# Kernel optimization log

Measured on AMD Instinct MI355X. Metric: run time of the kernel, lower is better.

The kernel has to match this reference:

```python
import jax, jax.numpy as jnp
import numpy as np

B, S, D, H, T, R = 2, 2048, 768, 12, 64, 50
DH = D // H
EPS = 1e-12


def setup_inputs() -> dict:
    key = jax.random.key(0)
    ks = jax.random.split(key, 12)
    w = lambda k, shape: jax.random.normal(k, shape, jnp.float32) * 0.02
    inp = {
        "hidden_states": jax.random.normal(ks[0], (B, S, D), jnp.float32),
        "tag_emb": w(ks[1], (T, D)),
        "sa_wq": w(ks[2], (D, D)), "sa_bq": jnp.zeros((D,), jnp.float32),
        "sa_wk": w(ks[3], (D, D)), "sa_bk": jnp.zeros((D,), jnp.float32),
        "sa_wv": w(ks[4], (D, D)), "sa_bv": jnp.zeros((D,), jnp.float32),
        "sa_wo": w(ks[5], (D, D)), "sa_bo": jnp.zeros((D,), jnp.float32),
        "sa_ln_g": jnp.ones((D,), jnp.float32), "sa_ln_b": jnp.zeros((D,), jnp.float32),
        "ca_wq": w(ks[6], (D, D)), "ca_bq": jnp.zeros((D,), jnp.float32),
        "ca_wk": w(ks[7], (D, D)), "ca_bk": jnp.zeros((D,), jnp.float32),
        "ca_wv": w(ks[8], (D, D)), "ca_bv": jnp.zeros((D,), jnp.float32),
        "ca_wo": w(ks[9], (D, D)), "ca_bo": jnp.zeros((D,), jnp.float32),
        "ca_ln_g": jnp.ones((D,), jnp.float32), "ca_ln_b": jnp.zeros((D,), jnp.float32),
        "ff_w1": w(ks[10], (D, 3072)), "ff_b1": jnp.zeros((3072,), jnp.float32),
        "ff_w2": w(ks[11], (3072, D)), "ff_b2": jnp.zeros((D,), jnp.float32),
        "ff_ln_g": jnp.ones((D,), jnp.float32), "ff_ln_b": jnp.zeros((D,), jnp.float32),
    }
    return inp


def _layernorm(x, g, b):
    m = jnp.mean(x, axis=-1, keepdims=True)
    v = jnp.mean(jnp.square(x - m), axis=-1, keepdims=True)
    return (x - m) * jax.lax.rsqrt(v + EPS) * g + b


def _bert_attention(x, kv, mask, wq, bq, wk, bk, wv, bv, wo, bo, ln_g, ln_b):
    # BertSelfAttention: multi-head attn; mask (if any) is ADDED to scores (HF semantics).
    Bq, Sq = x.shape[0], x.shape[1]
    Sk = kv.shape[1]
    q = (x @ wq + bq).reshape(Bq, Sq, H, DH)
    k = (kv @ wk + bk).reshape(Bq, Sk, H, DH)
    v = (kv @ wv + bv).reshape(Bq, Sk, H, DH)
    scores = jnp.einsum("bqhd,bkhd->bhqk", q, k) / jnp.sqrt(jnp.float32(DH))
    if mask is not None:
        scores = scores + mask  # additive 0/1 band mask, as in the source
    probs = jax.nn.softmax(scores, axis=-1)
    ctx = jnp.einsum("bhqk,bkhd->bqhd", probs, v).reshape(Bq, Sq, D)
    # BertSelfOutput: dense + residual + LayerNorm
    return _layernorm(ctx @ wo + bo + x, ln_g, ln_b)


def reference(hidden_states, tag_emb,
              sa_wq, sa_bq, sa_wk, sa_bk, sa_wv, sa_bv, sa_wo, sa_bo, sa_ln_g, sa_ln_b,
              ca_wq, ca_bq, ca_wk, ca_bk, ca_wv, ca_bv, ca_wo, ca_bo, ca_ln_g, ca_ln_b,
              ff_w1, ff_b1, ff_w2, ff_b2, ff_ln_g, ff_ln_b):
    Sd = hidden_states.shape[1]
    # banded mask: tril(+R) * triu(-R) -> 1 inside window, 0 outside (added to scores)
    i = jnp.arange(Sd)
    band = (jnp.abs(i[:, None] - i[None, :]) <= R).astype(hidden_states.dtype)  # [S,S]
    attn_out = _bert_attention(hidden_states, hidden_states, band,
                               sa_wq, sa_bq, sa_wk, sa_bk, sa_wv, sa_bv,
                               sa_wo, sa_bo, sa_ln_g, sa_ln_b)
    tags = jnp.broadcast_to(tag_emb[None], (hidden_states.shape[0], T, D))
    attn_out = _bert_attention(attn_out, tags, None,
                               ca_wq, ca_bq, ca_wk, ca_bk, ca_wv, ca_bv,
                               ca_wo, ca_bo, ca_ln_g, ca_ln_b)
    # BertIntermediate + BertOutput (exact erf gelu as in HF)
    inter = jax.nn.gelu(attn_out @ ff_w1 + ff_b1, approximate=False)
    return _layernorm(inter @ ff_w2 + ff_b2 + attn_out, ff_ln_g, ff_ln_b)
```

## Files before the change

kernel.cpp:

```cpp
#include <hip/hip_runtime.h>
#include <cstdint>
#include <cstddef>


typedef __bf16 bf16;
typedef __bf16 bf16x8 __attribute__((ext_vector_type(8)));
typedef __bf16 bf16x4 __attribute__((ext_vector_type(4)));
typedef __bf16 bf16x2 __attribute__((ext_vector_type(2)));
typedef float  floatx4 __attribute__((ext_vector_type(4)));

__device__ __forceinline__ void glds16(const bf16* g, bf16* l) {
  __builtin_amdgcn_global_load_lds((const __attribute__((address_space(1))) void*)g,
                                   (__attribute__((address_space(3))) void*)l, 16, 0, 0);
}

__device__ __forceinline__ float fexp2(float x) {
  float r;
  asm("v_exp_f32 %0, %1" : "=v"(r) : "v"(x));
  return r;
}

__global__ __launch_bounds__(256) void k_concat3(const float* __restrict__ a,
                                                 const float* __restrict__ b,
                                                 const float* __restrict__ c,
                                                 float* __restrict__ o, int seg) {
  int i = blockIdx.x * 256 + threadIdx.x;
  int s = i / seg, j = i - s * seg;
  const float* p = s == 0 ? a : (s == 1 ? b : c);
  o[i] = p[j];
}

__global__ void k_pad_tags(const float* __restrict__ tag, bf16* __restrict__ out) {
  int i = blockIdx.x * 256 + threadIdx.x;
  if (i < 64 * 768) out[i] = (bf16)tag[i];
  else if (i < 128 * 768) out[i] = (bf16)0.f;
}

__global__ __launch_bounds__(256) void k_transpose(const float* __restrict__ W,
                                                   bf16* __restrict__ Wt,
                                                   int K, int N) {
  __shared__ bf16 tile[64][72];
  int n0 = blockIdx.x * 64, k0 = blockIdx.y * 64;
  int t = threadIdx.x;
  int r = t >> 2, cg = (t & 3) * 16;
  const float* src = W + (size_t)(k0 + r) * N + n0 + cg;
  float tmp[16];
  *(float4*)&tmp[0]  = *(const float4*)(src);
  *(float4*)&tmp[4]  = *(const float4*)(src + 4);
  *(float4*)&tmp[8]  = *(const float4*)(src + 8);
  *(float4*)&tmp[12] = *(const float4*)(src + 12);
#pragma unroll
  for (int i = 0; i < 16; ++i) tile[r][cg + i] = (bf16)tmp[i];
  __syncthreads();
  bf16* dst = Wt + (size_t)(n0 + r) * K + k0 + cg;
#pragma unroll
  for (int g = 0; g < 2; ++g) {
    bf16x8 pack;
#pragma unroll
    for (int i = 0; i < 8; ++i) pack[i] = tile[cg + g * 8 + i][r];
    *(bf16x8*)(dst + g * 8) = pack;
  }
}

__global__ __launch_bounds__(256) void k_transpose4(const float* __restrict__ W0,
                                                    const float* __restrict__ W1,
                                                    const float* __restrict__ W2w,
                                                    const float* __restrict__ W3,
                                                    bf16* __restrict__ Wt) {
  __shared__ bf16 tile[64][72];
  int z = blockIdx.z;
  const float* W = z == 0 ? W0 : (z == 1 ? W1 : (z == 2 ? W2w : W3));
  bf16* dstb = Wt + (size_t)z * 768 * 768;
  int n0 = blockIdx.x * 64, k0 = blockIdx.y * 64;
  int t = threadIdx.x;
  int r = t >> 2, cg = (t & 3) * 16;
  const float* src = W + (size_t)(k0 + r) * 768 + n0 + cg;
  float tmp[16];
  *(float4*)&tmp[0]  = *(const float4*)(src);
  *(float4*)&tmp[4]  = *(const float4*)(src + 4);
  *(float4*)&tmp[8]  = *(const float4*)(src + 8);
  *(float4*)&tmp[12] = *(const float4*)(src + 12);
#pragma unroll
  for (int i = 0; i < 16; ++i) tile[r][cg + i] = (bf16)tmp[i];
  __syncthreads();
  bf16* dst = dstb + (size_t)(n0 + r) * 768 + k0 + cg;
#pragma unroll
  for (int g = 0; g < 2; ++g) {
    bf16x8 pack;
#pragma unroll
    for (int i = 0; i < 8; ++i) pack[i] = tile[cg + g * 8 + i][r];
    *(bf16x8*)(dst + g * 8) = pack;
  }
}

template <int BM, int KS, bool AF32, bool CF32>
__global__ __launch_bounds__(256) void k_gemm(const void* __restrict__ Av,
                                              const bf16* __restrict__ Bt,
                                              const float* __restrict__ bias,
                                              void* __restrict__ Cv,
                                              int M, int N, int K, int act) {
  constexpr int MT = BM / 32;
  __shared__ bf16 As[KS][BM * 32];
  __shared__ bf16 Bs[KS][128 * 32];
  int tid = threadIdx.x;
  int lane = tid & 63, wave = tid >> 6;
  int l16 = lane & 15, quad = lane >> 4;
  int wm = wave & 1, wn = wave >> 1;
  int m0 = blockIdx.x * BM, n0 = blockIdx.y * 128;
  int arow = tid >> 2, acol = (tid & 3) * 8;
  int ldst = arow * 32 + acol;

  const bf16* Ab = (const bf16*)Av;
  const float* Af = (const float*)Av;
  const bf16* Ap = Ab + (size_t)(m0 + arow) * K + acol;
  const float* Apf = Af + (size_t)(m0 + arow) * K + acol;
  const bf16* Bp = Bt + (size_t)(n0 + arow) * K + acol;

  floatx4 acc[MT][4];
#pragma unroll
  for (int i = 0; i < MT; ++i)
#pragma unroll
    for (int j = 0; j < 4; ++j) acc[i][j] = floatx4{0.f, 0.f, 0.f, 0.f};

  float4 p0a, p0b, p1a, p1b;
  if constexpr (AF32) {
    p0a = *(const float4*)(Apf);
    p0b = *(const float4*)(Apf + 4);
    p1a = *(const float4*)(Apf + (size_t)64 * K);
    p1b = *(const float4*)(Apf + (size_t)64 * K + 4);
  }

  for (int k = 0; k < K; k += 32 * KS) {
    __syncthreads();
#pragma unroll
    for (int ks = 0; ks < KS; ++ks) {
      glds16(Bp + k + ks * 32, &Bs[ks][ldst]);
      glds16(Bp + (size_t)64 * K + k + ks * 32, &Bs[ks][ldst + 2048]);
    }
    if constexpr (AF32) {
      bf16x8 c0, c1;
      c0[0] = (bf16)p0a.x; c0[1] = (bf16)p0a.y; c0[2] = (bf16)p0a.z; c0[3] = (bf16)p0a.w;
      c0[4] = (bf16)p0b.x; c0[5] = (bf16)p0b.y; c0[6] = (bf16)p0b.z; c0[7] = (bf16)p0b.w;
      c1[0] = (bf16)p1a.x; c1[1] = (bf16)p1a.y; c1[2] = (bf16)p1a.z; c1[3] = (bf16)p1a.w;
      c1[4] = (bf16)p1b.x; c1[5] = (bf16)p1b.y; c1[6] = (bf16)p1b.z; c1[7] = (bf16)p1b.w;
      *(bf16x8*)&As[0][ldst] = c0;
      *(bf16x8*)&As[0][ldst + 2048] = c1;
    } else {
#pragma unroll
      for (int ks = 0; ks < KS; ++ks) {
        glds16(Ap + k + ks * 32, &As[ks][ldst]);
        if constexpr (BM == 128) glds16(Ap + (size_t)64 * K + k + ks * 32, &As[ks][ldst + 2048]);
      }
    }
    __syncthreads();
    if constexpr (AF32) {
      if (k + 32 < K) {
        p0a = *(const float4*)(Apf + k + 32);
        p0b = *(const float4*)(Apf + k + 36);
        p1a = *(const float4*)(Apf + (size_t)64 * K + k + 32);
        p1b = *(const float4*)(Apf + (size_t)64 * K + k + 36);
      }
    }
#pragma unroll
    for (int ks = 0; ks < KS; ++ks) {
      bf16x8 a_frag[MT], b_frag[4];
#pragma unroll
      for (int mt = 0; mt < MT; ++mt)
        a_frag[mt] = *(const bf16x8*)&As[ks][(wm * (BM / 2) + mt * 16 + l16) * 32 + quad * 8];
#pragma unroll
      for (int nt = 0; nt < 4; ++nt)
        b_frag[nt] = *(const bf16x8*)&Bs[ks][(wn * 64 + nt * 16 + l16) * 32 + quad * 8];
#pragma unroll
      for (int mt = 0; mt < MT; ++mt)
#pragma unroll
        for (int nt = 0; nt < 4; ++nt)
          acc[mt][nt] = __builtin_amdgcn_mfma_f32_16x16x32_bf16(a_frag[mt], b_frag[nt], acc[mt][nt], 0, 0, 0);
    }
  }

#pragma unroll
  for (int nt = 0; nt < 4; ++nt) {
    int col = n0 + wn * 64 + nt * 16 + l16;
    float bv = bias[col];
#pragma unroll
    for (int mt = 0; mt < MT; ++mt) {
#pragma unroll
      for (int r = 0; r < 4; ++r) {
        int row = m0 + wm * (BM / 2) + mt * 16 + quad * 4 + r;
        float v = acc[mt][nt][r] + bv;
        if (act) v = 0.5f * v * (1.f + erff(v * 0.70710678118654752f));
        if constexpr (CF32) ((float*)Cv)[(size_t)row * N + col] = v;
        else ((bf16*)Cv)[(size_t)row * N + col] = (bf16)v;
      }
    }
  }
}

__global__ __launch_bounds__(256) void k_attn_mfma(const bf16* __restrict__ Q, int ldq,
                                                   const bf16* __restrict__ Kp,
                                                   const bf16* __restrict__ Vp, int ldkv,
                                                   bf16* __restrict__ O,
                                                   int S, int Skv,
                                                   long long kv_bstride, int bandR) {
  const int NH = 12;
  int qt = blockIdx.x, bh = blockIdx.y;
  int bb = bh / NH, h = bh % NH;
  const bf16* Qb = Q + (size_t)bb * S * ldq + h * 64;
  const bf16* Kb = Kp + (size_t)bb * kv_bstride + h * 64;
  const bf16* Vb = Vp + (size_t)bb * kv_bstride + h * 64;
  bf16* Ob = O + (size_t)bb * S * 768 + h * 64;

  __shared__ __align__(16) char smem[28672];
  bf16 (*Ks)[72] = (bf16(*)[72])(smem);
  bf16 (*Vt)[72] = (bf16(*)[72])(smem + 9216);
  float* Obuf = (float*)smem;
  float* l0_arr = (float*)(smem + 16896);

  int tid = threadIdx.x, wave = tid >> 6, lane = tid & 63;
  int quad = lane >> 4, l16 = lane & 15;
  int qh = wave & 1, kh = wave >> 1;
  bf16 (*Psw)[40] = (bf16(*)[40])(smem + 18432 + wave * 2560);

  const float C1 = 0.18033688f;
  const float C2 = 1.44269504f;

  int r = tid >> 2, cg = (tid & 3) * 16;
  int vk0 = 2 * (tid & 31);
  int vd0 = 8 * (tid >> 5);
  int vcol = (vk0 + 16 * (vd0 >> 4)) & 63;

  bf16x8 aq[2][2];
#pragma unroll
  for (int mt = 0; mt < 2; ++mt) {
    const bf16* qsrc = Qb + (size_t)(qt * 64 + qh * 32 + mt * 16 + l16) * ldq;
#pragma unroll
    for (int ks = 0; ks < 2; ++ks) {
      bf16x8 t = *(const bf16x8*)(qsrc + ks * 32 + quad * 8);
#pragma unroll
      for (int e = 0; e < 8; ++e) t[e] = (bf16)((float)t[e] * C1);
      aq[mt][ks] = t;
    }
  }

  bf16x8 kr0, kr1, vr0, vr1;
  {
    const bf16* ksrc = Kb + (size_t)r * ldkv + cg;
    kr0 = *(const bf16x8*)ksrc;
    kr1 = *(const bf16x8*)(ksrc + 8);
    const bf16* vsrc = Vb + (size_t)vk0 * ldkv + vd0;
    vr0 = *(const bf16x8*)vsrc;
    vr1 = *(const bf16x8*)(vsrc + ldkv);
  }

  float l_part[2][4];
  floatx4 acc[2][4];
#pragma unroll
  for (int mt = 0; mt < 2; ++mt)
#pragma unroll
    for (int j = 0; j < 4; ++j) {
      l_part[mt][j] = 0.f;
      acc[mt][j] = floatx4{0.f, 0.f, 0.f, 0.f};
    }

  int qi0 = qt * 64 + qh * 32 + quad * 4;

  for (int kc = 0; kc < Skv; kc += 64) {
    __syncthreads();
    *(bf16x8*)&Ks[r][cg] = kr0;
    *(bf16x8*)&Ks[r][cg + 8] = kr1;
#pragma unroll
    for (int e = 0; e < 8; ++e) {
      bf16x2 p; p[0] = vr0[e]; p[1] = vr1[e];
      *(bf16x2*)&Vt[vd0 + e][vcol] = p;
    }
    if (kc + 64 < Skv) {
      const bf16* ksrc = Kb + (size_t)(kc + 64 + r) * ldkv + cg;
      kr0 = *(const bf16x8*)ksrc;
      kr1 = *(const bf16x8*)(ksrc + 8);
      const bf16* vsrc = Vb + (size_t)(kc + 64 + vk0) * ldkv + vd0;
      vr0 = *(const bf16x8*)vsrc;
      vr1 = *(const bf16x8*)(vsrc + ldkv);
    }
    __syncthreads();

    floatx4 s[2][2];
#pragma unroll
    for (int kt = 0; kt < 2; ++kt) {
      bf16x8 bk0 = *(const bf16x8*)&Ks[kh * 32 + kt * 16 + l16][quad * 8];
      bf16x8 bk1 = *(const bf16x8*)&Ks[kh * 32 + kt * 16 + l16][32 + quad * 8];
#pragma unroll
      for (int mt = 0; mt < 2; ++mt) {
        floatx4 c = {0.f, 0.f, 0.f, 0.f};
        c = __builtin_amdgcn_mfma_f32_16x16x32_bf16(aq[mt][0], bk0, c, 0, 0, 0);
        c = __builtin_amdgcn_mfma_f32_16x16x32_bf16(aq[mt][1], bk1, c, 0, 0, 0);
        s[mt][kt] = c;
      }
    }

    bool masked = (bandR >= 0) && (kc <= qt * 64 + 63 + bandR) &&
                  (kc + 63 >= qt * 64 - bandR);
    if (masked) {
#pragma unroll
      for (int kt = 0; kt < 2; ++kt) {
        int kj = kc + kh * 32 + kt * 16 + l16;
        int colp = (kt * 16 + l16 + 8 * quad) & 31;
#pragma unroll
        for (int mt = 0; mt < 2; ++mt)
#pragma unroll
          for (int rr = 0; rr < 4; ++rr) {
            int d = qi0 + mt * 16 + rr - kj; if (d < 0) d = -d;
            float e = fexp2(s[mt][kt][rr] + (d <= bandR ? C2 : 0.f));
            l_part[mt][rr] += e;
            Psw[mt * 16 + quad * 4 + rr][colp] = (bf16)e;
          }
      }
    } else {
#pragma unroll
      for (int kt = 0; kt < 2; ++kt) {
        int colp = (kt * 16 + l16 + 8 * quad) & 31;
#pragma unroll
        for (int mt = 0; mt < 2; ++mt)
#pragma unroll
          for (int rr = 0; rr < 4; ++rr) {
            float e = fexp2(s[mt][kt][rr]);
            l_part[mt][rr] += e;
            Psw[mt * 16 + quad * 4 + rr][colp] = (bf16)e;
          }
      }
    }

    bf16x8 ap[2];
#pragma unroll
    for (int mt = 0; mt < 2; ++mt)
      ap[mt] = *(const bf16x8*)&Psw[mt * 16 + l16][8 * ((quad + (l16 >> 2)) & 3)];
#pragma unroll
    for (int nt = 0; nt < 4; ++nt) {
      bf16x8 bv = *(const bf16x8*)&Vt[nt * 16 + l16][(kh * 32 + quad * 8 + 16 * nt) & 63];
#pragma unroll
      for (int mt = 0; mt < 2; ++mt)
        acc[mt][nt] = __builtin_amdgcn_mfma_f32_16x16x32_bf16(ap[mt], bv, acc[mt][nt], 0, 0, 0);
    }
  }

  float lr[2][4];
#pragma unroll
  for (int mt = 0; mt < 2; ++mt)
#pragma unroll
    for (int rr = 0; rr < 4; ++rr) {
      float t = l_part[mt][rr];
      t += __shfl_xor(t, 1);
      t += __shfl_xor(t, 2);
      t += __shfl_xor(t, 4);
      t += __shfl_xor(t, 8);
      lr[mt][rr] = t;
    }
  __syncthreads();
  if (kh == 0) {
#pragma unroll
    for (int mt = 0; mt < 2; ++mt)
#pragma unroll
      for (int nt = 0; nt < 4; ++nt)
#pragma unroll
        for (int rr = 0; rr < 4; ++rr)
          Obuf[(qh * 32 + mt * 16 + quad * 4 + rr) * 66 + nt * 16 + l16] = acc[mt][nt][rr];
    if (l16 == 0) {
#pragma unroll
      for (int mt = 0; mt < 2; ++mt)
#pragma unroll
        for (int rr = 0; rr < 4; ++rr)
          l0_arr[qh * 32 + mt * 16 + quad * 4 + rr] = lr[mt][rr];
    }
  }
  __syncthreads();
  if (kh == 1) {
#pragma unroll
    for (int mt = 0; mt < 2; ++mt)
#pragma unroll
      for (int rr = 0; rr < 4; ++rr) {
        int ql = qh * 32 + mt * 16 + quad * 4 + rr;
        float lt = lr[mt][rr] + l0_arr[ql];
        int qrow = qt * 64 + ql;
#pragma unroll
        for (int nt = 0; nt < 4; ++nt) {
          float o = (acc[mt][nt][rr] + Obuf[ql * 66 + nt * 16 + l16]) / lt;
          Ob[(size_t)qrow * 768 + nt * 16 + l16] = (bf16)o;
        }
      }
  }
}

template <typename TY, typename TR, typename TO>
__global__ __launch_bounds__(256) void k_add_ln(const TY* __restrict__ Y,
                                                const TR* __restrict__ X,
                                                const float* __restrict__ g,
                                                const float* __restrict__ b,
                                                TO* __restrict__ out) {
  int wave = threadIdx.x >> 6, lane = threadIdx.x & 63;
  int row = blockIdx.x * 4 + wave;
  const TY* y = Y + (size_t)row * 768;
  const TR* x = X + (size_t)row * 768;
  float v[12];
  float s = 0.f, s2 = 0.f;
#pragma unroll
  for (int c = 0; c < 3; ++c) {
    int idx = c * 256 + lane * 4;
    float yv[4], xv[4];
    if constexpr (__is_same(TY, float)) {
      float4 t = *(const float4*)(y + idx);
      yv[0] = t.x; yv[1] = t.y; yv[2] = t.z; yv[3] = t.w;
    } else {
      bf16x4 t = *(const bf16x4*)(y + idx);
#pragma unroll
      for (int i = 0; i < 4; ++i) yv[i] = (float)t[i];
    }
    if constexpr (__is_same(TR, float)) {
      float4 t = *(const float4*)(x + idx);
      xv[0] = t.x; xv[1] = t.y; xv[2] = t.z; xv[3] = t.w;
    } else {
      bf16x4 t = *(const bf16x4*)(x + idx);
#pragma unroll
      for (int i = 0; i < 4; ++i) xv[i] = (float)t[i];
    }
#pragma unroll
    for (int i = 0; i < 4; ++i) {
      float t = yv[i] + xv[i];
      v[c * 4 + i] = t; s += t; s2 += t * t;
    }
  }
#pragma unroll
  for (int off = 32; off > 0; off >>= 1) { s += __shfl_xor(s, off); s2 += __shfl_xor(s2, off); }
  float mean = s * (1.f / 768.f);
  float var = fmaxf(s2 * (1.f / 768.f) - mean * mean, 0.f);
  float inv = rsqrtf(var + 1e-12f);
  TO* o = out + (size_t)row * 768;
#pragma unroll
  for (int c = 0; c < 3; ++c) {
    int idx = c * 256 + lane * 4;
    float4 gv = *(const float4*)(g + idx);
    float4 bv = *(const float4*)(b + idx);
    float r0 = (v[c * 4 + 0] - mean) * inv * gv.x + bv.x;
    float r1 = (v[c * 4 + 1] - mean) * inv * gv.y + bv.y;
    float r2 = (v[c * 4 + 2] - mean) * inv * gv.z + bv.z;
    float r3 = (v[c * 4 + 3] - mean) * inv * gv.w + bv.w;
    if constexpr (__is_same(TO, float)) {
      float4 ov = {r0, r1, r2, r3};
      *(float4*)(o + idx) = ov;
    } else {
      bf16x4 ov;
      ov[0] = (bf16)r0; ov[1] = (bf16)r1; ov[2] = (bf16)r2; ov[3] = (bf16)r3;
      *(bf16x4*)(o + idx) = ov;
    }
  }
}

extern "C" void kernel_launch(void* const* d_in, const int* in_sizes, int n_in,
                              void* d_out, int out_size, void* d_ws, size_t ws_size,
                              hipStream_t stream) {
  (void)in_sizes; (void)n_in; (void)out_size; (void)ws_size;
  const float* X     = (const float*)d_in[0];
  const float* tag   = (const float*)d_in[1];
  const float* sa_wq = (const float*)d_in[2];
  const float* sa_bq = (const float*)d_in[3];
  const float* sa_wk = (const float*)d_in[4];
  const float* sa_bk = (const float*)d_in[5];
  const float* sa_wv = (const float*)d_in[6];
  const float* sa_bv = (const float*)d_in[7];
  const float* sa_wo = (const float*)d_in[8];
  const float* sa_bo = (const float*)d_in[9];
  const float* sa_lg = (const float*)d_in[10];
  const float* sa_lb = (const float*)d_in[11];
  const float* ca_wq = (const float*)d_in[12];
  const float* ca_bq = (const float*)d_in[13];
  const float* ca_wk = (const float*)d_in[14];
  const float* ca_bk = (const float*)d_in[15];
  const float* ca_wv = (const float*)d_in[16];
  const float* ca_bv = (const float*)d_in[17];
  const float* ca_wo = (const float*)d_in[18];
  const float* ca_bo = (const float*)d_in[19];
  const float* ca_lg = (const float*)d_in[20];
  const float* ca_lb = (const float*)d_in[21];
  const float* ff_w1 = (const float*)d_in[22];
  const float* ff_b1 = (const float*)d_in[23];
  const float* ff_w2 = (const float*)d_in[24];
  const float* ff_b2 = (const float*)d_in[25];
  const float* ff_lg = (const float*)d_in[26];
  const float* ff_lb = (const float*)d_in[27];

  float* outf = (float*)d_out;
  bf16* outb = (bf16*)d_out;
  const size_t SLOT = (size_t)4096 * 768;

  bf16* BIG   = (bf16*)d_ws;
  bf16* slotA = BIG + (size_t)4096 * 2304;
  bf16* Wall  = slotA + SLOT;
  bf16* W2    = Wall + (size_t)3072 * 768;
  bf16* tagp  = W2;
  bf16* k2v2  = W2 + (size_t)128 * 768;
  float* bQKV = (float*)(W2 + (size_t)128 * 768 + (size_t)128 * 1536);
  float* bKV2 = bQKV + 2304;

  dim3 blk(256);

  k_concat3<<<dim3(9), blk, 0, stream>>>(sa_bq, sa_bk, sa_bv, bQKV, 768);
  k_concat3<<<dim3(6), blk, 0, stream>>>(ca_bk, ca_bv, nullptr, bKV2, 768);
  k_pad_tags<<<dim3(384), blk, 0, stream>>>(tag, tagp);

  k_transpose4<<<dim3(12, 12, 4), blk, 0, stream>>>(sa_wq, sa_wk, sa_wv, sa_wo, Wall);
  k_gemm<128, 1, true, false><<<dim3(32, 18), blk, 0, stream>>>(X, Wall, bQKV, BIG,
                                                                4096, 2304, 768, 0);
  k_attn_mfma<<<dim3(32, 24), blk, 0, stream>>>(BIG, 2304, BIG + 768, BIG + 1536, 2304,
                                                outb, 2048, 2048, (long long)2048 * 2304, 50);
  k_gemm<64, 2, false, false><<<dim3(64, 6), blk, 0, stream>>>(outb, Wall + (size_t)2304 * 768,
                                                               sa_bo, slotA, 4096, 768, 768, 0);
  k_add_ln<bf16, float, bf16><<<dim3(1024), blk, 0, stream>>>(slotA, X, sa_lg, sa_lb, slotA);

  k_transpose4<<<dim3(12, 12, 4), blk, 0, stream>>>(ca_wq, ca_wk, ca_wv, ca_wo, Wall);
  k_gemm<64, 2, false, false><<<dim3(64, 6), blk, 0, stream>>>(slotA, Wall, ca_bq, BIG,
                                                               4096, 768, 768, 0);
  k_gemm<64, 2, false, false><<<dim3(2, 12), blk, 0, stream>>>(tagp, Wall + (size_t)768 * 768,
                                                               bKV2, k2v2, 128, 1536, 768, 0);
  k_attn_mfma<<<dim3(32, 24), blk, 0, stream>>>(BIG, 768, k2v2, k2v2 + 768, 1536,
                                                outb, 2048, 64, 0, -1);
  k_gemm<64, 2, false, false><<<dim3(64, 6), blk, 0, stream>>>(outb, Wall + (size_t)2304 * 768,
                                                               ca_bo, BIG + SLOT, 4096, 768, 768, 0);
  k_add_ln<bf16, bf16, bf16><<<dim3(1024), blk, 0, stream>>>(BIG + SLOT, slotA, ca_lg, ca_lb, slotA);

  k_transpose<<<dim3(48, 12), blk, 0, stream>>>(ff_w1, Wall, 768, 3072);
  k_transpose<<<dim3(12, 48), blk, 0, stream>>>(ff_w2, W2, 3072, 768);
  for (int mc = 0; mc < 2; ++mc) {
    const bf16* a2 = slotA + (size_t)mc * 2048 * 768;
    float* yo = outf + (size_t)mc * 2048 * 768;
    k_gemm<128, 2, false, false><<<dim3(16, 24), blk, 0, stream>>>(a2, Wall, ff_b1, BIG,
                                                                   2048, 3072, 768, 1);
    k_gemm<64, 2, false, true><<<dim3(32, 6), blk, 0, stream>>>(BIG, W2, ff_b2, yo,
                                                                2048, 768, 3072, 0);
    k_add_ln<float, bf16, float><<<dim3(512), blk, 0, stream>>>(yo, a2, ff_lg, ff_lb, yo);
  }
}
```

Baseline: 468.1 us.

## Split self-attention over two KV halves and merge partial results

The banded self-attention kernel gains a third grid dimension that splits the 2048-key range into two halves. Each half writes its unnormalized partial output, stored as bf16, into its own slab of the output buffer and its row sums into a new Lbuf. A new merge kernel then adds the two partials and divides by the combined row sum. This doubles the number of attention blocks to raise parallelism and shorten per-block work, at the cost of an extra kernel launch, extra global traffic for the partials, and extra rounding from storing unnormalized values in bf16.

```diff
diff --git a/kernel.cpp b/kernel.cpp
--- a/kernel.cpp
+++ b/kernel.cpp
@@ -200,15 +200,18 @@
                                                    const bf16* __restrict__ Kp,
                                                    const bf16* __restrict__ Vp, int ldkv,
                                                    bf16* __restrict__ O,
-                                                   int S, int Skv,
+                                                   float* __restrict__ Lbuf,
+                                                   int S, int kvlen,
                                                    long long kv_bstride, int bandR) {
   const int NH = 12;
-  int qt = blockIdx.x, bh = blockIdx.y;
+  int qt = blockIdx.x, bh = blockIdx.y, z = blockIdx.z;
   int bb = bh / NH, h = bh % NH;
+  int kv0 = z * kvlen;
   const bf16* Qb = Q + (size_t)bb * S * ldq + h * 64;
   const bf16* Kb = Kp + (size_t)bb * kv_bstride + h * 64;
   const bf16* Vb = Vp + (size_t)bb * kv_bstride + h * 64;
-  bf16* Ob = O + (size_t)bb * S * 768 + h * 64;
+  size_t slab = (size_t)z * (size_t)(gridDim.y / NH) * S * 768;
+  bf16* Ob = O + slab + (size_t)bb * S * 768 + h * 64;
 
   __shared__ __align__(16) char smem[28672];
   bf16 (*Ks)[72] = (bf16(*)[72])(smem);
@@ -244,10 +247,10 @@
 
   bf16x8 kr0, kr1, vr0, vr1;
   {
-    const bf16* ksrc = Kb + (size_t)r * ldkv + cg;
+    const bf16* ksrc = Kb + (size_t)(kv0 + r) * ldkv + cg;
     kr0 = *(const bf16x8*)ksrc;
     kr1 = *(const bf16x8*)(ksrc + 8);
-    const bf16* vsrc = Vb + (size_t)vk0 * ldkv + vd0;
+    const bf16* vsrc = Vb + (size_t)(kv0 + vk0) * ldkv + vd0;
     vr0 = *(const bf16x8*)vsrc;
     vr1 = *(const bf16x8*)(vsrc + ldkv);
   }
@@ -263,8 +266,9 @@
     }
 
   int qi0 = qt * 64 + qh * 32 + quad * 4;
-
-  for (int kc = 0; kc < Skv; kc += 64) {
+  int kv_end = kv0 + kvlen;
+
+  for (int kc = kv0; kc < kv_end; kc += 64) {
     __syncthreads();
     *(bf16x8*)&Ks[r][cg] = kr0;
     *(bf16x8*)&Ks[r][cg + 8] = kr1;
@@ -273,7 +277,7 @@
       bf16x2 p; p[0] = vr0[e]; p[1] = vr1[e];
       *(bf16x2*)&Vt[vd0 + e][vcol] = p;
     }
-    if (kc + 64 < Skv) {
+    if (kc + 64 < kv_end) {
       const bf16* ksrc = Kb + (size_t)(kc + 64 + r) * ldkv + cg;
       kr0 = *(const bf16x8*)ksrc;
       kr1 = *(const bf16x8*)(ksrc + 8);
@@ -380,13 +384,41 @@
         int ql = qh * 32 + mt * 16 + quad * 4 + rr;
         float lt = lr[mt][rr] + l0_arr[ql];
         int qrow = qt * 64 + ql;
-#pragma unroll
-        for (int nt = 0; nt < 4; ++nt) {
-          float o = (acc[mt][nt][rr] + Obuf[ql * 66 + nt * 16 + l16]) / lt;
-          Ob[(size_t)qrow * 768 + nt * 16 + l16] = (bf16)o;
+        if (Lbuf) {
+          if (l16 == 0)
+            Lbuf[((size_t)z * gridDim.y + bh) * S + qrow] = lt;
+#pragma unroll
+          for (int nt = 0; nt < 4; ++nt) {
+            float o = acc[mt][nt][rr] + Obuf[ql * 66 + nt * 16 + l16];
+            Ob[(size_t)qrow * 768 + nt * 16 + l16] = (bf16)o;
+          }
+        } else {
+#pragma unroll
+          for (int nt = 0; nt < 4; ++nt) {
+            float o = (acc[mt][nt][rr] + Obuf[ql * 66 + nt * 16 + l16]) / lt;
+            Ob[(size_t)qrow * 768 + nt * 16 + l16] = (bf16)o;
+          }
         }
       }
   }
+}
+
+__global__ __launch_bounds__(256) void k_attn_merge(bf16* __restrict__ O,
+                                                    const float* __restrict__ Lbuf) {
+  int i = blockIdx.x * 256 + threadIdx.x;
+  int r = i / 96;
+  int c = (i - r * 96) * 8;
+  size_t base = (size_t)r * 768 + c;
+  int bh = (r >> 11) * 12 + (c >> 6);
+  int row = r & 2047;
+  float l = Lbuf[(size_t)bh * 2048 + row] + Lbuf[(size_t)(24 + bh) * 2048 + row];
+  float inv = 1.f / l;
+  bf16x8 p0 = *(const bf16x8*)(O + base);
+  bf16x8 p1 = *(const bf16x8*)(O + (size_t)4096 * 768 + base);
+  bf16x8 o;
+#pragma unroll
+  for (int e = 0; e < 8; ++e) o[e] = (bf16)(((float)p0[e] + (float)p1[e]) * inv);
+  *(bf16x8*)(O + base) = o;
 }
 
 template <typename TY, typename TR, typename TO>
@@ -498,6 +530,7 @@
   bf16* k2v2  = W2 + (size_t)128 * 768;
   float* bQKV = (float*)(W2 + (size_t)128 * 768 + (size_t)128 * 1536);
   float* bKV2 = bQKV + 2304;
+  float* Lbuf = bKV2 + 1536;
 
   dim3 blk(256);
 
@@ -508,8 +541,10 @@
   k_transpose4<<<dim3(12, 12, 4), blk, 0, stream>>>(sa_wq, sa_wk, sa_wv, sa_wo, Wall);
   k_gemm<128, 1, true, false><<<dim3(32, 18), blk, 0, stream>>>(X, Wall, bQKV, BIG,
                                                                 4096, 2304, 768, 0);
-  k_attn_mfma<<<dim3(32, 24), blk, 0, stream>>>(BIG, 2304, BIG + 768, BIG + 1536, 2304,
-                                                outb, 2048, 2048, (long long)2048 * 2304, 50);
+  k_attn_mfma<<<dim3(32, 24, 2), blk, 0, stream>>>(BIG, 2304, BIG + 768, BIG + 1536, 2304,
+                                                   outb, Lbuf, 2048, 1024,
+                                                   (long long)2048 * 2304, 50);
+  k_attn_merge<<<dim3(1536), blk, 0, stream>>>(outb, Lbuf);
   k_gemm<64, 2, false, false><<<dim3(64, 6), blk, 0, stream>>>(outb, Wall + (size_t)2304 * 768,
                                                                sa_bo, slotA, 4096, 768, 768, 0);
   k_add_ln<bf16, float, bf16><<<dim3(1024), blk, 0, stream>>>(slotA, X, sa_lg, sa_lb, slotA);
@@ -519,8 +554,8 @@
                                                                4096, 768, 768, 0);
   k_gemm<64, 2, false, false><<<dim3(2, 12), blk, 0, stream>>>(tagp, Wall + (size_t)768 * 768,
                                                                bKV2, k2v2, 128, 1536, 768, 0);
-  k_attn_mfma<<<dim3(32, 24), blk, 0, stream>>>(BIG, 768, k2v2, k2v2 + 768, 1536,
-                                                outb, 2048, 64, 0, -1);
+  k_attn_mfma<<<dim3(32, 24, 1), blk, 0, stream>>>(BIG, 768, k2v2, k2v2 + 768, 1536,
+                                                   outb, nullptr, 2048, 64, 0, -1);
   k_gemm<64, 2, false, false><<<dim3(64, 6), blk, 0, stream>>>(outb, Wall + (size_t)2304 * 768,
                                                                ca_bo, BIG + SLOT, 4096, 768, 768, 0);
   k_add_ln<bf16, bf16, bf16><<<dim3(1024), blk, 0, stream>>>(BIG + SLOT, slotA, ca_lg, ca_lb, slotA);
```

Measured after the change: 472.4 us. No clear change (+0.9%).
